# Optimization experiments

Hardware: AMD Instinct MI355X
Metric: run time of the kernel (lower is better)

Reference implementation:

```python
import jax, jax.numpy as jnp
import numpy as np

H, D, K = 8, 64, 9           # new num heads, head size, conv kernel size
A = H * D                    # all_head_size = 512
HID = 2 * A                  # input hidden size = 1024
STD = 0.02


def setup_inputs() -> dict:
    key = jax.random.key(0)
    ks = jax.random.split(key, 16)
    B, S = 4, 2048
    f = jnp.float32
    inp = {
        'hidden_states': jax.random.normal(ks[0], (B, S, HID), f),
        'Wq': jax.random.normal(ks[1], (A, A), f) * STD,
        'bq': jnp.zeros((A,), f),
        'Wk': jax.random.normal(ks[2], (A, A), f) * STD,
        'bk': jnp.zeros((A,), f),
        'Wv': jax.random.normal(ks[3], (A, A), f) * STD,
        'bv': jnp.zeros((A,), f),
        'dw_w': jax.random.normal(ks[4], (A, 1, K), f) * STD,   # depthwise conv (groups=A)
        'pw_w': jax.random.normal(ks[5], (A, A, 1), f) * STD,   # pointwise 1x1 conv
        'sep_b': jnp.zeros((A, 1), f),                          # SeparableConv1D bias
        'Wck': jax.random.normal(ks[6], (H * K, A), f) * STD,   # conv_kernel_layer
        'bck': jnp.zeros((H * K,), f),
        'Wco': jax.random.normal(ks[7], (A, A), f) * STD,       # conv_out_layer
        'bco': jnp.zeros((A,), f),
    }
    return inp


def reference(hidden_states, Wq, bq, Wk, bk, Wv, bv, dw_w, pw_w, sep_b, Wck, bck, Wco, bco):
    B, S, _ = hidden_states.shape
    hs_attn = hidden_states[:, :, :A]
    hs_conv = hidden_states[:, :, A:]

    q = hs_attn @ Wq.T + bq
    k = hs_attn @ Wk.T + bk
    v = hs_attn @ Wv.T + bv

    # SeparableConv1D on (B, A, S): depthwise then pointwise, plus bias
    x = hs_conv.transpose(0, 2, 1)
    x = jax.lax.conv_general_dilated(
        x, dw_w, window_strides=(1,), padding=[(K // 2, K // 2)],
        feature_group_count=A, dimension_numbers=('NCH', 'OIH', 'NCH'))
    x = jnp.einsum('bcs,oc->bos', x, pw_w[:, :, 0]) + sep_b
    mixed_key_conv = x.transpose(0, 2, 1)            # (B,S,A)

    # per-token softmax conv kernel
    conv_attn = mixed_key_conv * hs_conv
    ckl = (conv_attn @ Wck.T + bck).reshape(B, S, H, K)
    ckl = jax.nn.softmax(ckl, axis=-1)               # softmax over kernel taps

    # dynamic-span lightweight convolution (unfold -> batched matmul)
    col = hs_conv @ Wco.T + bco                      # (B,S,A)
    pad = jnp.pad(col, ((0, 0), (K // 2, K // 2), (0, 0)))
    windows = jnp.stack([pad[:, i:i + S] for i in range(K)], axis=-1)  # (B,S,A,K)
    windows = windows.reshape(B, S, H, D, K)
    conv_out = jnp.einsum('bshdk,bshk->bshd', windows, ckl)            # (B,S,H,D)

    # standard self-attention
    qh = q.reshape(B, S, H, D).transpose(0, 2, 1, 3)
    kh = k.reshape(B, S, H, D).transpose(0, 2, 1, 3)
    vh = v.reshape(B, S, H, D).transpose(0, 2, 1, 3)
    scale = jnp.asarray(1.0 / np.sqrt(D), q.dtype)
    scores = jnp.einsum('bhqd,bhkd->bhqk', qh, kh) * scale
    probs = jax.nn.softmax(scores, axis=-1)
    ctx = jnp.einsum('bhqk,bhkd->bqhd', probs, vh)   # (B,S,H,D)

    out = jnp.concatenate([ctx, conv_out], axis=2)   # (B,S,2H,D)
    return out.reshape(B, S, HID)
```

## Files before the change

kernel.cpp:

```cpp
#include <hip/hip_runtime.h>
#include <hip/hip_bf16.h>

#define NH   8
#define HD   64
#define KW   9
#define AD   512
#define HIDD 1024
#define BB   4
#define SS   2048
#define MTOK (BB*SS)
#define WSZ  262144

typedef __attribute__((ext_vector_type(8))) short short8;
typedef __attribute__((ext_vector_type(4))) float floatx4;

__device__ __forceinline__ short f2bf(float f) {
    unsigned u = __float_as_uint(f);
    u = (u + 0x7FFFu + ((u >> 16) & 1u)) >> 16;
    return (short)u;
}
__device__ __forceinline__ float bf2f(short s) {
    return __uint_as_float(((unsigned)(unsigned short)s) << 16);
}
__device__ __forceinline__ float exp2_raw(float x) {
    return __builtin_amdgcn_exp2f(x);
}
__device__ __forceinline__ unsigned pkbf2(float a, float b) {
    unsigned au = __float_as_uint(a) + 0x8000u;
    unsigned bu = __float_as_uint(b) + 0x8000u;
    return __builtin_amdgcn_perm(bu, au, 0x07060302);
}
__device__ __forceinline__ void gl2lds16(const short* g, short* l) {
    __builtin_amdgcn_global_load_lds(
        (const __attribute__((address_space(1))) void*)g,
        (__attribute__((address_space(3))) void*)l, 16, 0, 0);
}

__global__ __launch_bounds__(256) void cvt_hs_kernel(
    const float* __restrict__ hs, short* __restrict__ hsb)
{
    int idx = blockIdx.x * 256 + threadIdx.x;
    const float* s = hs + (long)idx * 8;
    float4 a = *(const float4*)s, c = *(const float4*)(s + 4);
    short8 o;
    o[0]=f2bf(a.x); o[1]=f2bf(a.y); o[2]=f2bf(a.z); o[3]=f2bf(a.w);
    o[4]=f2bf(c.x); o[5]=f2bf(c.y); o[6]=f2bf(c.z); o[7]=f2bf(c.w);
    *(short8*)(hsb + (long)idx * 8) = o;
}

__global__ __launch_bounds__(256) void cvt_w_kernel(
    const float* __restrict__ pw, const float* __restrict__ Wco,
    const float* __restrict__ Wq, const float* __restrict__ Wk,
    const float* __restrict__ Wv, const float* __restrict__ Wck,
    const float* __restrict__ dw,
    short* __restrict__ dst, float* __restrict__ dwT)
{
    int idx = blockIdx.x * 256 + threadIdx.x;
    if (idx >= 172032) {
        int t = idx - 172032;
        if (t < AD * KW) {
            int c = t / KW, k = t - c * KW;
            dwT[k * AD + c] = dw[t];
        }
        return;
    }
    int e0 = idx * 8;
    short8 o;
    if (e0 < 5 * WSZ) {
        int w = e0 >> 18, off = e0 & (WSZ - 1);
        const float* src = (w == 0) ? pw : (w == 1) ? Wco : (w == 2) ? Wq
                         : (w == 3) ? Wk : Wv;
        float4 a = *(const float4*)(src + off), c = *(const float4*)(src + off + 4);
        o[0]=f2bf(a.x); o[1]=f2bf(a.y); o[2]=f2bf(a.z); o[3]=f2bf(a.w);
        o[4]=f2bf(c.x); o[5]=f2bf(c.y); o[6]=f2bf(c.z); o[7]=f2bf(c.w);
    } else {
        int off = e0 - 5 * WSZ;
        int row = off >> 9, col = off & 511;
        if (row < NH * KW) {
            const float* src = Wck + row * AD + col;
            float4 a = *(const float4*)src, c = *(const float4*)(src + 4);
            o[0]=f2bf(a.x); o[1]=f2bf(a.y); o[2]=f2bf(a.z); o[3]=f2bf(a.w);
            o[4]=f2bf(c.x); o[5]=f2bf(c.y); o[6]=f2bf(c.z); o[7]=f2bf(c.w);
        } else {
            for (int i = 0; i < 8; ++i) o[i] = 0;
        }
    }
    *(short8*)(dst + e0) = o;
}

__global__ __launch_bounds__(256) void dwconv_kernel(
    const short* __restrict__ hsb, const float* __restrict__ dwT,
    short* __restrict__ x1)
{
    int idx = blockIdx.x * 256 + threadIdx.x;
    int c8  = (idx & 63) * 8;
    int tok = idx >> 6;
    int s   = tok & (SS - 1);
    int b   = tok >> 11;
    const short* base = hsb + (long)(b * SS) * HIDD + AD + c8;
    float acc[8];
#pragma unroll
    for (int i = 0; i < 8; ++i) acc[i] = 0.f;
#pragma unroll
    for (int kk = 0; kk < KW; ++kk) {
        int ss2 = s + kk - KW / 2;
        if (ss2 >= 0 && ss2 < SS) {
            short8 hv = *(const short8*)(base + (long)ss2 * HIDD);
            float4 w0 = *(const float4*)(dwT + kk * AD + c8);
            float4 w1 = *(const float4*)(dwT + kk * AD + c8 + 4);
            acc[0] += w0.x * bf2f(hv[0]); acc[1] += w0.y * bf2f(hv[1]);
            acc[2] += w0.z * bf2f(hv[2]); acc[3] += w0.w * bf2f(hv[3]);
            acc[4] += w1.x * bf2f(hv[4]); acc[5] += w1.y * bf2f(hv[5]);
            acc[6] += w1.z * bf2f(hv[6]); acc[7] += w1.w * bf2f(hv[7]);
        }
    }
    short8 o;
#pragma unroll
    for (int i = 0; i < 8; ++i) o[i] = f2bf(acc[i]);
    *(short8*)(x1 + (long)tok * AD + c8) = o;
}

template<int FM, int FN, int MODE>
__global__ __launch_bounds__(256) void gemm_bf16_kernel(
    const short* __restrict__ X, int ldx, int xoff,
    const short* __restrict__ W,
    const float* __restrict__ b0p, const float* __restrict__ b1p,
    const float* __restrict__ b2p,
    const short* __restrict__ mulp, int mul_ld, int mul_off,
    void* __restrict__ Cout, short* __restrict__ vtout,
    int ldc, int N, int Kd, float oscale)
{
    constexpr int TM = 32 * FM, TN = 32 * FN;
    __shared__ __align__(16) short As[TM * 64];
    __shared__ __align__(16) short Bs[TN * 64];
    const int tid  = threadIdx.x;
    const int wv   = tid >> 6, lane = tid & 63;
    const int ln   = lane & 15, quad = lane >> 4;
    const int wm   = wv >> 1, wn = wv & 1;
    const int m0 = blockIdx.x * TM, n0 = blockIdx.y * TN;

    floatx4 acc[FM][FN];
#pragma unroll
    for (int i = 0; i < FM; ++i)
#pragma unroll
        for (int j = 0; j < FN; ++j) acc[i][j] = (floatx4){0.f, 0.f, 0.f, 0.f};

    const short* xbase = X + (long)m0 * ldx + xoff;
    const short* wbase = W + (long)n0 * Kd;

    for (int k0 = 0; k0 < Kd; k0 += 64) {
#pragma unroll
        for (int g = tid; g < TM * 8; g += 256) {
            int m = g >> 3, p = g & 7, gk = p ^ (m & 7);
            gl2lds16(xbase + (long)m * ldx + k0 + gk * 8, &As[g * 8]);
        }
#pragma unroll
        for (int g = tid; g < TN * 8; g += 256) {
            int m = g >> 3, p = g & 7, gk = p ^ (m & 7);
            gl2lds16(wbase + (long)m * Kd + k0 + gk * 8, &Bs[g * 8]);
        }
        __syncthreads();
#pragma unroll
        for (int half = 0; half < 2; ++half) {
            short8 afr[FM], bfr[FN];
#pragma unroll
            for (int i = 0; i < FM; ++i) {
                int p = (half * 4 + quad) ^ (ln & 7);
                afr[i] = *(const short8*)&As[(wm * 16 * FM + i * 16 + ln) * 64 + p * 8];
            }
#pragma unroll
            for (int j = 0; j < FN; ++j) {
                int p = (half * 4 + quad) ^ (ln & 7);
                bfr[j] = *(const short8*)&Bs[(wn * 16 * FN + j * 16 + ln) * 64 + p * 8];
            }
#pragma unroll
            for (int i = 0; i < FM; ++i)
#pragma unroll
                for (int j = 0; j < FN; ++j)
                    acc[i][j] = __builtin_amdgcn_mfma_f32_16x16x32_bf16(
                        afr[i], bfr[j], acc[i][j], 0, 0, 0);
        }
        __syncthreads();
    }

#pragma unroll
    for (int j = 0; j < FN; ++j) {
        int n = n0 + wn * 16 * FN + j * 16 + ln;
        if constexpr (MODE == 3) {
            if (n >= 1024) {
                int hh = (n - 1024) >> 6, dd = (n - 1024) & 63;
                float bv = b2p[n - 1024];
                int mblk = m0 + wm * 16 * FM;
                int bidx = mblk >> 11, sblk = mblk & (SS - 1);
                short* dst = vtout + ((long)((bidx * NH + hh) * HD + dd)) * SS + sblk;
#pragma unroll
                for (int r = 0; r < 4; ++r) {
                    unsigned lo = pkbf2(acc[0][j][r] + bv, acc[1 % FM][j][r] + bv);
                    unsigned hi = pkbf2(acc[2 % FM][j][r] + bv, acc[3 % FM][j][r] + bv);
                    *(uint2*)(dst + (quad * 4 + r) * 4) = make_uint2(lo, hi);
                }
            } else {
                float bv = (n < 512) ? b0p[n] : b1p[n - 512];
                float sc = (n < 512) ? oscale : 1.f;
#pragma unroll
                for (int i = 0; i < FM; ++i) {
#pragma unroll
                    for (int r = 0; r < 4; ++r) {
                        int m = m0 + wm * 16 * FM + i * 16 + quad * 4 + r;
                        float val = (acc[i][j][r] + bv) * sc;
                        ((short*)Cout)[(long)m * ldc + n] = f2bf(val);
                    }
                }
            }
        } else if (n < N) {
            float bv = b0p[n], sc = oscale;
#pragma unroll
            for (int i = 0; i < FM; ++i) {
#pragma unroll
                for (int r = 0; r < 4; ++r) {
                    int m = m0 + wm * 16 * FM + i * 16 + quad * 4 + r;
                    float val = (acc[i][j][r] + bv) * sc;
                    if constexpr (MODE == 2)
                        val *= bf2f(mulp[(long)m * mul_ld + mul_off + n]);
                    if constexpr (MODE == 0)
                        ((float*)Cout)[(long)m * ldc + n] = val;
                    else
                        ((short*)Cout)[(long)m * ldc + n] = f2bf(val);
                }
            }
        }
    }
}

__global__ __launch_bounds__(256) void convout_kernel(
    const short* __restrict__ col, const float* __restrict__ ckl,
    float* __restrict__ out)
{
    int idx = blockIdx.x * 256 + threadIdx.x;
    int d4  = (idx & 127) * 4;
    int tok = idx >> 7;
    int s   = tok & (SS - 1);
    int b   = tok >> 11;
    int h   = d4 >> 6;
    const float* lg = ckl + (long)tok * (NH * KW) + h * KW;
    float wv[KW];
    float mx = -1e30f;
#pragma unroll
    for (int i = 0; i < KW; ++i) { wv[i] = lg[i]; mx = fmaxf(mx, wv[i]); }
    float sum = 0.f;
#pragma unroll
    for (int i = 0; i < KW; ++i) { wv[i] = __expf(wv[i] - mx); sum += wv[i]; }
    float inv = 1.f / sum;
    float a0 = 0.f, a1 = 0.f, a2 = 0.f, a3 = 0.f;
    const short* cbase = col + (long)(b * SS) * AD + d4;
#pragma unroll
    for (int kk = 0; kk < KW; ++kk) {
        int ss2 = s + kk - KW / 2;
        if (ss2 >= 0 && ss2 < SS) {
            uint2 cv = *(const uint2*)(cbase + (long)ss2 * AD);
            float w = wv[kk];
            a0 += w * bf2f((short)(cv.x & 0xFFFF));
            a1 += w * bf2f((short)(cv.x >> 16));
            a2 += w * bf2f((short)(cv.y & 0xFFFF));
            a3 += w * bf2f((short)(cv.y >> 16));
        }
    }
    *(float4*)&out[(long)tok * HIDD + AD + d4] =
        make_float4(a0 * inv, a1 * inv, a2 * inv, a3 * inv);
}

__global__ __launch_bounds__(256) void flash_mfma_kernel(
    const short* __restrict__ qkv, const short* __restrict__ vT,
    float* __restrict__ out)
{
    const int qt = blockIdx.x, h = blockIdx.y, b = blockIdx.z;
    const int tid  = threadIdx.x;
    const int w    = tid >> 6;
    const int lane = tid & 63;
    const int ln   = lane & 15;
    const int quad = lane >> 4;

    __shared__ __align__(16) short Kb[64 * 64];
    __shared__ __align__(16) short Vt[64 * 64];
    __shared__ __align__(16) short Ps[4][16 * 72];

    const int  q0 = qt * 64;
    const long rowbase = (long)b * SS;

    short8 qa[2];
    {
        const short* qrow = qkv + (rowbase + q0 + w * 16 + ln) * 1536 + h * HD;
        qa[0] = *(const short8*)(qrow + quad * 8);
        qa[1] = *(const short8*)(qrow + 32 + quad * 8);
    }

    floatx4 acc[4];
    float l_i[4];
#pragma unroll
    for (int r = 0; r < 4; ++r) {
        l_i[r] = 0.f;
        acc[r] = (floatx4){0.f, 0.f, 0.f, 0.f};
    }

    const short* kbase  = qkv + 512 + rowbase * 1536 + h * HD;
    const short* vtbase = vT + ((long)(b * NH + h) * HD) * SS;

    for (int kt = 0; kt < SS / 64; ++kt) {
        const int k0 = kt * 64;
#pragma unroll
        for (int it = 0; it < 2; ++it) {
            int g = it * 256 + tid;
            int m = g >> 3, p = g & 7, gk = p ^ (m & 7);
            gl2lds16(kbase + (long)(k0 + m) * 1536 + gk * 8, &Kb[g * 8]);
        }
#pragma unroll
        for (int it = 0; it < 2; ++it) {
            int g = it * 256 + tid;
            int m = g >> 3, p = g & 7, gk = p ^ (m & 7);
            gl2lds16(vtbase + (long)m * SS + k0 + gk * 8, &Vt[g * 8]);
        }
        __syncthreads();

        floatx4 S[4];
#pragma unroll
        for (int st = 0; st < 4; ++st) {
            int p0i = quad ^ (ln & 7), p1i = (4 + quad) ^ (ln & 7);
            short8 b0 = *(const short8*)&Kb[(st * 16 + ln) * 64 + p0i * 8];
            short8 b1 = *(const short8*)&Kb[(st * 16 + ln) * 64 + p1i * 8];
            floatx4 z = (floatx4){0.f, 0.f, 0.f, 0.f};
            z = __builtin_amdgcn_mfma_f32_16x16x32_bf16(qa[0], b0, z, 0, 0, 0);
            S[st] = __builtin_amdgcn_mfma_f32_16x16x32_bf16(qa[1], b1, z, 0, 0, 0);
        }

#pragma unroll
        for (int r = 0; r < 4; ++r) {
            float p0 = exp2_raw(S[0][r]);
            float p1 = exp2_raw(S[1][r]);
            float p2 = exp2_raw(S[2][r]);
            float p3 = exp2_raw(S[3][r]);
            l_i[r] += (p0 + p1) + (p2 + p3);
            unsigned lo = pkbf2(p0, p1);
            unsigned hi = pkbf2(p2, p3);
            *(uint2*)&Ps[w][(quad * 4 + r) * 72 + ln * 4] = make_uint2(lo, hi);
        }

        {
            short8 pa0 = *(const short8*)&Ps[w][ln * 72 + quad * 8];
            short8 pa1 = *(const short8*)&Ps[w][ln * 72 + 32 + quad * 8];
#pragma unroll
            for (int st = 0; st < 4; ++st) {
                int p0i = quad ^ (ln & 7), p1i = (4 + quad) ^ (ln & 7);
                short8 vb0 = *(const short8*)&Vt[(st * 16 + ln) * 64 + p0i * 8];
                short8 vb1 = *(const short8*)&Vt[(st * 16 + ln) * 64 + p1i * 8];
                acc[st] = __builtin_amdgcn_mfma_f32_16x16x32_bf16(pa0, vb0, acc[st], 0, 0, 0);
                acc[st] = __builtin_amdgcn_mfma_f32_16x16x32_bf16(pa1, vb1, acc[st], 0, 0, 0);
            }
        }
        __syncthreads();
    }

#pragma unroll
    for (int r = 0; r < 4; ++r) {
#pragma unroll
        for (int off = 1; off < 16; off <<= 1)
            l_i[r] += __shfl_xor(l_i[r], off);
    }

#pragma unroll
    for (int r = 0; r < 4; ++r) {
        float inv = 1.f / l_i[r];
        float* orow = out + (rowbase + q0 + w * 16 + quad * 4 + r) * HIDD + h * HD;
#pragma unroll
        for (int st = 0; st < 4; ++st)
            orow[st * 16 + ln] = acc[st][r] * inv;
    }
}

extern "C" void kernel_launch(void* const* d_in, const int* in_sizes, int n_in,
                              void* d_out, int out_size, void* d_ws, size_t ws_size,
                              hipStream_t stream)
{
    const float* hs   = (const float*)d_in[0];
    const float* Wq   = (const float*)d_in[1];
    const float* bq   = (const float*)d_in[2];
    const float* Wk   = (const float*)d_in[3];
    const float* bk   = (const float*)d_in[4];
    const float* Wv   = (const float*)d_in[5];
    const float* bv   = (const float*)d_in[6];
    const float* dw   = (const float*)d_in[7];
    const float* pw   = (const float*)d_in[8];
    const float* sepb = (const float*)d_in[9];
    const float* Wck  = (const float*)d_in[10];
    const float* bck  = (const float*)d_in[11];
    const float* Wco  = (const float*)d_in[12];
    const float* bco  = (const float*)d_in[13];
    float* out = (float*)d_out;

    short* hsb  = (short*)d_ws;
    short* x1c  = hsb + (long)MTOK * HIDD;
    short* qkvb = x1c + (long)MTOK * AD;
    short* vTb  = qkvb + (long)MTOK * 1536;
    float* ckl  = (float*)(vTb + (long)MTOK * AD);
    short* wb   = (short*)(ckl + (long)MTOK * (NH * KW));
    short* pw_b   = wb;
    short* Wco_b  = wb + 1L * WSZ;
    short* Wqkv_b = wb + 2L * WSZ;
    short* Wck_b  = wb + 5L * WSZ;
    float* dwT    = (float*)(Wck_b + 128L * AD);
    short* cab    = qkvb;

    const float QSCALE = 0.18033688011112042f;

    cvt_hs_kernel<<<MTOK * HIDD / 2048, 256, 0, stream>>>(hs, hsb);
    cvt_w_kernel<<<690, 256, 0, stream>>>(
        pw, Wco, Wq, Wk, Wv, Wck, dw, wb, dwT);
    dwconv_kernel<<<MTOK * AD / 2048, 256, 0, stream>>>(hsb, dwT, x1c);
    gemm_bf16_kernel<2, 2, 2><<<dim3(MTOK / 64, AD / 64), 256, 0, stream>>>(
        x1c, AD, 0, pw_b, sepb, nullptr, nullptr, hsb, HIDD, AD,
        cab, nullptr, AD, AD, AD, 1.f);
    gemm_bf16_kernel<2, 2, 0><<<dim3(MTOK / 64, 2), 256, 0, stream>>>(
        cab, AD, 0, Wck_b, bck, nullptr, nullptr, nullptr, 0, 0,
        ckl, nullptr, NH * KW, NH * KW, AD, 1.f);
    gemm_bf16_kernel<2, 2, 1><<<dim3(MTOK / 64, AD / 64), 256, 0, stream>>>(
        hsb, HIDD, AD, Wco_b, bco, nullptr, nullptr, nullptr, 0, 0,
        x1c, nullptr, AD, AD, AD, 1.f);
    convout_kernel<<<MTOK * AD / 1024, 256, 0, stream>>>(x1c, ckl, out);
    gemm_bf16_kernel<4, 4, 3><<<dim3(MTOK / 128, 1536 / 128), 256, 0, stream>>>(
        hsb, HIDD, 0, Wqkv_b, bq, bk, bv, nullptr, 0, 0,
        qkvb, vTb, 1536, 1536, AD, QSCALE);
    flash_mfma_kernel<<<dim3(SS / 64, NH, BB), 256, 0, stream>>>(qkvb, vTb, out);

    (void)in_sizes; (void)n_in; (void)out_size; (void)ws_size;
}
```

Before: 229.7 us.

## Overlap K/V tile loads with compute using split-phase barriers in attention loop

Restructures the flash-attention inner loop so the next K tile is fetched into LDS while the PV phase waits on V, and the next V tile is fetched while QK^T runs. It uses raw s_barrier with explicit vmcnt waits instead of __syncthreads, and precomputes the load addresses as incrementing pointers. The intent is to hide global-to-LDS latency behind MFMA work. It relies on vmcnt ordering and raw barriers being correct, which adds correctness risk and more barriers per iteration.

```diff
diff --git a/kernel.cpp b/kernel.cpp
--- a/kernel.cpp
+++ b/kernel.cpp
@@ -302,25 +302,26 @@
         acc[r] = (floatx4){0.f, 0.f, 0.f, 0.f};
     }
 
+    const int m1 = tid >> 3,  gk1 = (tid & 7) ^ (m1 & 7);
+    const int g2 = 256 + tid;
+    const int m2 = g2 >> 3,   gk2 = (g2 & 7) ^ (m2 & 7);
     const short* kbase  = qkv + 512 + rowbase * 1536 + h * HD;
     const short* vtbase = vT + ((long)(b * NH + h) * HD) * SS;
-
-    for (int kt = 0; kt < SS / 64; ++kt) {
-        const int k0 = kt * 64;
-#pragma unroll
-        for (int it = 0; it < 2; ++it) {
-            int g = it * 256 + tid;
-            int m = g >> 3, p = g & 7, gk = p ^ (m & 7);
-            gl2lds16(kbase + (long)(k0 + m) * 1536 + gk * 8, &Kb[g * 8]);
-        }
-#pragma unroll
-        for (int it = 0; it < 2; ++it) {
-            int g = it * 256 + tid;
-            int m = g >> 3, p = g & 7, gk = p ^ (m & 7);
-            gl2lds16(vtbase + (long)m * SS + k0 + gk * 8, &Vt[g * 8]);
-        }
-        __syncthreads();
-
+    const short* sk0 = kbase  + (long)m1 * 1536 + gk1 * 8;
+    const short* sk1 = kbase  + (long)m2 * 1536 + gk2 * 8;
+    const short* sv0 = vtbase + (long)m1 * SS   + gk1 * 8;
+    const short* sv1 = vtbase + (long)m2 * SS   + gk2 * 8;
+    short* const dk0 = &Kb[tid * 8];
+    short* const dk1 = &Kb[g2 * 8];
+    short* const dv0 = &Vt[tid * 8];
+    short* const dv1 = &Vt[g2 * 8];
+
+#define STAGE_K() do { gl2lds16(sk0, dk0); gl2lds16(sk1, dk1); \
+                       sk0 += 64 * 1536; sk1 += 64 * 1536; } while (0)
+#define STAGE_V() do { gl2lds16(sv0, dv0); gl2lds16(sv1, dv1); \
+                       sv0 += 64; sv1 += 64; } while (0)
+
+    auto qkt_phase = [&]() {
         floatx4 S[4];
 #pragma unroll
         for (int st = 0; st < 4; ++st) {
@@ -331,7 +332,6 @@
             z = __builtin_amdgcn_mfma_f32_16x16x32_bf16(qa[0], b0, z, 0, 0, 0);
             S[st] = __builtin_amdgcn_mfma_f32_16x16x32_bf16(qa[1], b1, z, 0, 0, 0);
         }
-
 #pragma unroll
         for (int r = 0; r < 4; ++r) {
             float p0 = exp2_raw(S[0][r]);
@@ -343,21 +343,52 @@
             unsigned hi = pkbf2(p2, p3);
             *(uint2*)&Ps[w][(quad * 4 + r) * 72 + ln * 4] = make_uint2(lo, hi);
         }
-
-        {
-            short8 pa0 = *(const short8*)&Ps[w][ln * 72 + quad * 8];
-            short8 pa1 = *(const short8*)&Ps[w][ln * 72 + 32 + quad * 8];
-#pragma unroll
-            for (int st = 0; st < 4; ++st) {
-                int p0i = quad ^ (ln & 7), p1i = (4 + quad) ^ (ln & 7);
-                short8 vb0 = *(const short8*)&Vt[(st * 16 + ln) * 64 + p0i * 8];
-                short8 vb1 = *(const short8*)&Vt[(st * 16 + ln) * 64 + p1i * 8];
-                acc[st] = __builtin_amdgcn_mfma_f32_16x16x32_bf16(pa0, vb0, acc[st], 0, 0, 0);
-                acc[st] = __builtin_amdgcn_mfma_f32_16x16x32_bf16(pa1, vb1, acc[st], 0, 0, 0);
-            }
-        }
-        __syncthreads();
-    }
+    };
+
+    auto pv_phase = [&]() {
+        short8 pa0 = *(const short8*)&Ps[w][ln * 72 + quad * 8];
+        short8 pa1 = *(const short8*)&Ps[w][ln * 72 + 32 + quad * 8];
+#pragma unroll
+        for (int st = 0; st < 4; ++st) {
+            int p0i = quad ^ (ln & 7), p1i = (4 + quad) ^ (ln & 7);
+            short8 vb0 = *(const short8*)&Vt[(st * 16 + ln) * 64 + p0i * 8];
+            short8 vb1 = *(const short8*)&Vt[(st * 16 + ln) * 64 + p1i * 8];
+            acc[st] = __builtin_amdgcn_mfma_f32_16x16x32_bf16(pa0, vb0, acc[st], 0, 0, 0);
+            acc[st] = __builtin_amdgcn_mfma_f32_16x16x32_bf16(pa1, vb1, acc[st], 0, 0, 0);
+        }
+    };
+
+    STAGE_K();
+    STAGE_V();
+    asm volatile("s_waitcnt vmcnt(0)" ::: "memory");
+    __builtin_amdgcn_s_barrier();
+    asm volatile("" ::: "memory");
+
+    const int NT = SS / 64;
+    for (int kt = 0; kt < NT - 1; ++kt) {
+        qkt_phase();
+        __builtin_amdgcn_s_barrier();
+        asm volatile("" ::: "memory");
+        STAGE_K();
+        asm volatile("s_waitcnt vmcnt(2)" ::: "memory");
+        __builtin_amdgcn_s_barrier();
+        asm volatile("" ::: "memory");
+        pv_phase();
+        __builtin_amdgcn_s_barrier();
+        asm volatile("" ::: "memory");
+        STAGE_V();
+        asm volatile("s_waitcnt vmcnt(2)" ::: "memory");
+        __builtin_amdgcn_s_barrier();
+        asm volatile("" ::: "memory");
+    }
+    qkt_phase();
+    asm volatile("s_waitcnt vmcnt(0)" ::: "memory");
+    __builtin_amdgcn_s_barrier();
+    asm volatile("" ::: "memory");
+    pv_phase();
+
+#undef STAGE_K
+#undef STAGE_V
 
 #pragma unroll
     for (int r = 0; r < 4; ++r) {
```

New measurement: 223.3 us. 1.03x faster.
